# Optimization experiments

Hardware: AMD Instinct MI355X
Metric: run time of the kernel (lower is better)

## Reference

```python
import jax, jax.numpy as jnp
import numpy as np

B, S, D = 2, 2048, 1024  # batch, seq, model_dim
E, K, H = 8, 2, 4096     # experts, top_k, expert hidden
CAP_FACTOR = 1.0


def setup_inputs() -> dict:
    key = jax.random.key(0)
    ks = jax.random.split(key, 6)
    scale_in = 1.0 / np.sqrt(D)
    scale_h = 1.0 / np.sqrt(H)
    return {
        "x": jax.random.normal(ks[0], (B, S, D), jnp.float32),
        "wg": jax.random.normal(ks[1], (D, E), jnp.float32) * scale_in,
        "w1": jax.random.normal(ks[2], (E, D, H), jnp.float32) * scale_in,
        "b1": jnp.zeros((E, H), jnp.float32),
        "w2": jax.random.normal(ks[3], (E, H, D), jnp.float32) * scale_h,
        "b2": jnp.zeros((E, D), jnp.float32),
    }


def _moe_forward(x, wg, w1, b1, w2, b2):
    Bb, Ss, Dd = x.shape
    T = Bb * Ss
    cap = int(K * CAP_FACTOR * ((T + E - 1) // E))  # Tutel capacity rule
    xt = x.reshape(T, Dd)

    # ---- gating ----
    logits = xt @ wg                      # [T, E]
    scores = jax.nn.softmax(logits, axis=-1)
    gates_k, idx_k = jax.lax.top_k(scores, K)  # [T, K]
    # normalize_gate=True: renormalize top-k gates
    gates_k = gates_k / jnp.sum(gates_k, axis=-1, keepdims=True)

    # ---- GShard-style location assignment (slot-major cumsum) ----
    masks = jax.nn.one_hot(idx_k, E, dtype=jnp.int32)           # [T, K, E]
    m = jnp.transpose(masks, (1, 0, 2)).reshape(K * T, E)       # slot-major
    locs_full = jnp.cumsum(m, axis=0) - 1                       # [K*T, E]
    loc = jnp.sum(locs_full * m, axis=-1)                       # [K*T]
    loc = loc.reshape(K, T).T                                   # [T, K]
    valid = (loc < cap).astype(xt.dtype)                        # capacity drop
    loc_c = jnp.clip(loc, 0, cap - 1)

    # ---- dispatch: scatter tokens into [E, cap, D] ----
    contrib = (xt[:, None, :] * valid[:, :, None]).reshape(T * K, Dd)
    disp = jnp.zeros((E, cap, Dd), xt.dtype)
    disp = disp.at[idx_k.reshape(-1), loc_c.reshape(-1)].add(contrib)

    # ---- grouped expert FFN ----
    h = jax.nn.relu(jnp.einsum("ecd,edh->ech", disp, w1) + b1[:, None, :])
    out = jnp.einsum("ech,ehd->ecd", h, w2) + b2[:, None, :]

    # ---- combine (postscore): gather + gate-weighted sum ----
    gathered = out[idx_k, loc_c]                                # [T, K, D]
    y = jnp.einsum("tk,tkd->td", gates_k * valid, gathered)
    return y.reshape(Bb, Ss, Dd)


def reference(x, wg, w1, b1, w2, b2):
    return _moe_forward(x, wg, w1, b1, w2, b2)
```

## Files before the change

### kernel.cpp

```cpp
#include <hip/hip_runtime.h>
#include <stdint.h>

#define NTOK 4096
#define DIM  1024
#define NEXP 8
#define HID  4096
#define CAP  1024

typedef __bf16 bf16x8 __attribute__((ext_vector_type(8)));
typedef float  f32x4  __attribute__((ext_vector_type(4)));

__device__ __forceinline__ unsigned short f2bf(float f) {
  unsigned int u = __float_as_uint(f);
  return (unsigned short)((u + 0x7fffu + ((u >> 16) & 1u)) >> 16);
}

__device__ __forceinline__ float bf2f(unsigned int bits16) {
  return __uint_as_float(bits16 << 16);
}

__device__ __forceinline__ void load_lds16(const void* g, void* l) {
  __builtin_amdgcn_global_load_lds(
      (__attribute__((address_space(1))) void*)g,
      (__attribute__((address_space(3))) void*)l,
      16, 0, 0);
}

__global__ void gating_kernel(const float* __restrict__ x, const float* __restrict__ wg,
                              int* __restrict__ tok_e, float* __restrict__ tok_g) {
  const int t = blockIdx.x;
  const int l = threadIdx.x;
  float acc[NEXP];
#pragma unroll
  for (int e = 0; e < NEXP; ++e) acc[e] = 0.f;

  const float4* x4  = (const float4*)(x + (size_t)t * DIM);
  const float4* wg4 = (const float4*)wg;
#pragma unroll
  for (int i = 0; i < 4; ++i) {
    int dq = i * 64 + l;
    float4 xv = x4[dq];
    float xs[4] = {xv.x, xv.y, xv.z, xv.w};
#pragma unroll
    for (int c = 0; c < 4; ++c) {
      int d = dq * 4 + c;
      float4 wa = wg4[d * 2], wb = wg4[d * 2 + 1];
      acc[0] += xs[c] * wa.x; acc[1] += xs[c] * wa.y;
      acc[2] += xs[c] * wa.z; acc[3] += xs[c] * wa.w;
      acc[4] += xs[c] * wb.x; acc[5] += xs[c] * wb.y;
      acc[6] += xs[c] * wb.z; acc[7] += xs[c] * wb.w;
    }
  }
#pragma unroll
  for (int off = 32; off; off >>= 1)
#pragma unroll
    for (int e = 0; e < NEXP; ++e) acc[e] += __shfl_xor(acc[e], off);

  if (l == 0) {
    float m = acc[0];
#pragma unroll
    for (int e = 1; e < NEXP; ++e) m = fmaxf(m, acc[e]);
    float p[NEXP];
#pragma unroll
    for (int e = 0; e < NEXP; ++e) p[e] = __expf(acc[e] - m);
    int e0 = 0; float b0 = p[0];
#pragma unroll
    for (int e = 1; e < NEXP; ++e) if (p[e] > b0) { b0 = p[e]; e0 = e; }
    int e1 = -1; float b1v = -1.f;
#pragma unroll
    for (int e = 0; e < NEXP; ++e) if (e != e0 && p[e] > b1v) { b1v = p[e]; e1 = e; }
    float inv = 1.f / (b0 + b1v);
    tok_e[2 * t] = e0; tok_e[2 * t + 1] = e1;
    tok_g[2 * t] = b0 * inv; tok_g[2 * t + 1] = b1v * inv;
  }
}

__global__ void scan_kernel(const int* __restrict__ tok_e, int* __restrict__ tok_loc,
                            int* __restrict__ slot_map) {
  const int l = threadIdx.x;
  const unsigned long long below = (1ull << l) - 1ull;
  int base[NEXP];
#pragma unroll
  for (int e = 0; e < NEXP; ++e) base[e] = 0;

  int nxt = tok_e[((0 * 64 + l) & (NTOK - 1)) * 2 + ((0 * 64 + l) >> 12)];
  for (int it = 0; it < 128; ++it) {
    int e = nxt;
    if (it + 1 < 128) {
      int g2 = (it + 1) * 64 + l;
      nxt = tok_e[(g2 & (NTOK - 1)) * 2 + (g2 >> 12)];
    }
    int loc = 0;
#pragma unroll
    for (int ex = 0; ex < NEXP; ++ex) {
      unsigned long long msk = __ballot(e == ex);
      int off = __popcll(msk & below);
      if (e == ex) loc = base[ex] + off;
      base[ex] += __popcll(msk);
    }
    int g = it * 64 + l;
    int k = g >> 12, t = g & (NTOK - 1);
    bool valid = loc < CAP;
    tok_loc[t * 2 + k] = valid ? loc : -1;
    if (valid) slot_map[e * CAP + loc] = t;
  }
#pragma unroll
  for (int ex = 0; ex < NEXP; ++ex) {
    int c = base[ex] < CAP ? base[ex] : CAP;
    for (int i = c + l; i < CAP; i += 64) slot_map[ex * CAP + i] = -1;
  }
}

__global__ void dispatch_kernel(const float* __restrict__ x, const int* __restrict__ slot_map,
                                unsigned short* __restrict__ disp) {
  const int s = blockIdx.x;
  const int tid = threadIdx.x;
  int t = slot_map[s];
  uint2 o;
  if (t >= 0) {
    float4 v = ((const float4*)(x + (size_t)t * DIM))[tid];
    o.x = (unsigned)f2bf(v.x) | ((unsigned)f2bf(v.y) << 16);
    o.y = (unsigned)f2bf(v.z) | ((unsigned)f2bf(v.w) << 16);
  } else {
    o.x = 0u; o.y = 0u;
  }
  ((uint2*)(disp + (size_t)s * DIM))[tid] = o;
}

__global__ void transpose_cvt(const float* __restrict__ in, unsigned short* __restrict__ out,
                              int R, int C) {
  __shared__ float tile[64][65];
  const int e = blockIdx.z;
  const float* inp = in + (size_t)e * R * C;
  unsigned short* outp = out + (size_t)e * R * C;
  const int c0 = blockIdx.x * 64, r0 = blockIdx.y * 64;
  const int t = threadIdx.x;
#pragma unroll
  for (int i = 0; i < 4; ++i) {
    int idx = i * 256 + t;
    int r = idx >> 4, c4 = (idx & 15) * 4;
    float4 v = *(const float4*)(inp + (size_t)(r0 + r) * C + c0 + c4);
    tile[r][c4 + 0] = v.x; tile[r][c4 + 1] = v.y;
    tile[r][c4 + 2] = v.z; tile[r][c4 + 3] = v.w;
  }
  __syncthreads();
#pragma unroll
  for (int i = 0; i < 2; ++i) {
    int idx = i * 256 + t;
    int c = idx >> 3, r8 = (idx & 7) * 8;
    unsigned short s[8];
#pragma unroll
    for (int j = 0; j < 8; ++j) s[j] = f2bf(tile[r8 + j][c]);
    uint4 o;
    o.x = (unsigned)s[0] | ((unsigned)s[1] << 16);
    o.y = (unsigned)s[2] | ((unsigned)s[3] << 16);
    o.z = (unsigned)s[4] | ((unsigned)s[5] << 16);
    o.w = (unsigned)s[6] | ((unsigned)s[7] << 16);
    *(uint4*)(outp + (size_t)(c0 + c) * R + r0 + r8) = o;
  }
}

template <bool RELU, int MB, int NB>
__global__ __launch_bounds__(256)
void gemm_kernel(const unsigned short* __restrict__ A, const unsigned short* __restrict__ B,
                 const float* __restrict__ bias, unsigned short* __restrict__ C,
                 int N, int K) {
  constexpr int M = 1024;
  const int bid = blockIdx.x;
  const int e = bid / (MB * NB);
  const int r = bid - e * (MB * NB);
  const int patch = r / (MB * 4);
  const int q = r - patch * (MB * 4);
  const int mtile = q >> 2;
  const int ntile = patch * 4 + (q & 3);

  A += (size_t)e * M * K;
  B += (size_t)e * N * K;
  bias += (size_t)e * N;
  C += (size_t)e * M * N;
  const int m0 = mtile * 128;
  const int n0 = ntile * 128;
  const int tid = threadIdx.x;
  const int wave = tid >> 6, lane = tid & 63;
  const int wm = wave >> 1, wn = wave & 1;

  __shared__ __align__(16) unsigned short As[128 * 64];
  __shared__ __align__(16) unsigned short Bs[128 * 64];

  const int srow = lane >> 3;
  const int scol = ((lane & 7) ^ (srow & 7)) * 8;
  const unsigned short* gA = A + (size_t)(m0 + wave * 8 + srow) * K + scol;
  const unsigned short* gB = B + (size_t)(n0 + wave * 8 + srow) * K + scol;
  const int lbase = (wave * 8) * 64;

  f32x4 acc[4][4] = {};

  const int quad = lane >> 4;
  const int lxor = lane & 7;
  const int arowb = (wm * 64 + (lane & 15)) * 64;
  const int browb = (wn * 64 + (lane & 15)) * 64;

  const int nIter = K >> 6;
  for (int it = 0; it < nIter; ++it) {
#pragma unroll
    for (int i = 0; i < 4; ++i) {
      load_lds16(gA + (size_t)i * 32 * K, &As[lbase + i * 32 * 64]);
      load_lds16(gB + (size_t)i * 32 * K, &Bs[lbase + i * 32 * 64]);
    }
    gA += 64; gB += 64;
    __syncthreads();
#pragma unroll
    for (int kk = 0; kk < 64; kk += 32) {
      const int coff = ((quad + (kk >> 3)) ^ lxor) * 8;
      bf16x8 af[4], bfr[4];
#pragma unroll
      for (int i = 0; i < 4; ++i)
        af[i] = *reinterpret_cast<const bf16x8*>(&As[arowb + i * 16 * 64 + coff]);
#pragma unroll
      for (int j = 0; j < 4; ++j)
        bfr[j] = *reinterpret_cast<const bf16x8*>(&Bs[browb + j * 16 * 64 + coff]);
#pragma unroll
      for (int i = 0; i < 4; ++i)
#pragma unroll
        for (int j = 0; j < 4; ++j)
          acc[i][j] = __builtin_amdgcn_mfma_f32_16x16x32_bf16(af[i], bfr[j], acc[i][j], 0, 0, 0);
    }
    __syncthreads();
  }

  unsigned short* scr = (wave < 2 ? As : Bs) + (wave & 1) * 2304;
  const int lc = lane & 15;
  const int erow = lane >> 3;
  const int ecol = (lane & 7) * 8;
  unsigned short* Cbase = C + (size_t)(m0 + wm * 64) * N + n0 + wn * 64;
#pragma unroll
  for (int h2 = 0; h2 < 2; ++h2) {
#pragma unroll
    for (int j = 0; j < 4; ++j) {
      float bj = bias[n0 + wn * 64 + j * 16 + lc];
#pragma unroll
      for (int ii = 0; ii < 2; ++ii) {
        int i = h2 * 2 + ii;
#pragma unroll
        for (int rr = 0; rr < 4; ++rr) {
          float v = acc[i][j][rr] + bj;
          if (RELU) v = fmaxf(v, 0.f);
          scr[(ii * 16 + quad * 4 + rr) * 72 + j * 16 + lc] = f2bf(v);
        }
      }
    }
    __asm__ volatile("s_waitcnt lgkmcnt(0)" ::: "memory");
#pragma unroll
    for (int p = 0; p < 4; ++p) {
      uint4 v = *(const uint4*)&scr[(p * 8 + erow) * 72 + ecol];
      *(uint4*)&Cbase[(size_t)(h2 * 32 + p * 8 + erow) * N + ecol] = v;
    }
  }
}

__global__ void combine_kernel(const unsigned short* __restrict__ outb,
                               const int* __restrict__ tok_e, const int* __restrict__ tok_loc,
                               const float* __restrict__ tok_g, float* __restrict__ y) {
  const int t = blockIdx.x;
  const int tid = threadIdx.x;
  int e0 = tok_e[2 * t], e1 = tok_e[2 * t + 1];
  int l0 = tok_loc[2 * t], l1 = tok_loc[2 * t + 1];
  float g0 = tok_g[2 * t], g1 = tok_g[2 * t + 1];
  float ax = 0.f, ay = 0.f, az = 0.f, aw = 0.f;
  if (l0 >= 0) {
    uint2 u = ((const uint2*)(outb + ((size_t)e0 * CAP + l0) * DIM))[tid];
    ax += g0 * bf2f(u.x & 0xffffu); ay += g0 * __uint_as_float(u.x & 0xffff0000u);
    az += g0 * bf2f(u.y & 0xffffu); aw += g0 * __uint_as_float(u.y & 0xffff0000u);
  }
  if (l1 >= 0) {
    uint2 u = ((const uint2*)(outb + ((size_t)e1 * CAP + l1) * DIM))[tid];
    ax += g1 * bf2f(u.x & 0xffffu); ay += g1 * __uint_as_float(u.x & 0xffff0000u);
    az += g1 * bf2f(u.y & 0xffffu); aw += g1 * __uint_as_float(u.y & 0xffff0000u);
  }
  float4 o; o.x = ax; o.y = ay; o.z = az; o.w = aw;
  ((float4*)(y + (size_t)t * DIM))[tid] = o;
}

extern "C" void kernel_launch(void* const* d_in, const int* in_sizes, int n_in,
                              void* d_out, int out_size, void* d_ws, size_t ws_size,
                              hipStream_t stream) {
  const float* x  = (const float*)d_in[0];
  const float* wg = (const float*)d_in[1];
  const float* w1 = (const float*)d_in[2];
  const float* b1 = (const float*)d_in[3];
  const float* w2 = (const float*)d_in[4];
  const float* b2 = (const float*)d_in[5];
  float* y = (float*)d_out;

  char* ws = (char*)d_ws;
  int*   tok_e    = (int*)(ws);
  int*   tok_loc  = (int*)(ws + 32768);
  float* tok_g    = (float*)(ws + 65536);
  int*   slot_map = (int*)(ws + 98304);
  unsigned short* disp = (unsigned short*)(ws + 131072);
  unsigned short* wbuf = (unsigned short*)(ws + 131072 + (16ull << 20));
  unsigned short* h    = (unsigned short*)(ws + 131072 + (80ull << 20));
  unsigned short* outb = (unsigned short*)(ws + 131072 + (144ull << 20));

  gating_kernel<<<NTOK, 64, 0, stream>>>(x, wg, tok_e, tok_g);
  scan_kernel<<<1, 64, 0, stream>>>(tok_e, tok_loc, slot_map);
  dispatch_kernel<<<NEXP * CAP, 256, 0, stream>>>(x, slot_map, disp);
  transpose_cvt<<<dim3(HID / 64, DIM / 64, NEXP), 256, 0, stream>>>(w1, wbuf, DIM, HID);
  gemm_kernel<true, 8, 32><<<NEXP * 8 * 32, 256, 0, stream>>>(disp, wbuf, b1, h, HID, DIM);
  transpose_cvt<<<dim3(DIM / 64, HID / 64, NEXP), 256, 0, stream>>>(w2, wbuf, HID, DIM);
  gemm_kernel<false, 8, 8><<<NEXP * 8 * 8, 256, 0, stream>>>(h, wbuf, b2, outb, DIM, HID);
  combine_kernel<<<NTOK, 256, 0, stream>>>(outb, tok_e, tok_loc, tok_g, y);
}
```

Before: 544.0 us.

## Fuse dispatch and weight fp32-to-bf16 transpose into expert GEMM loads

The separate dispatch kernel and the two weight transpose/convert kernels are removed. Each GEMM now loads fp32 weights directly and converts them to bf16 in registers before writing transposed tiles to LDS, and GEMM1 gathers token rows through slot_map. The scan is split across four waves using per-wave counts and prefix offsets. This avoids writing and re-reading bf16 copies of the weights and dispatched activations. The cost is that each GEMM tile re-reads and re-converts fp32 weights, which doubles global read bytes per tile, and global loads now go through registers with no async LDS path.

Result: slower. 625.3 us (+14.9%).

```diff
diff --git a/kernel.cpp b/kernel.cpp
--- a/kernel.cpp
+++ b/kernel.cpp
@@ -17,6 +17,10 @@
 
 __device__ __forceinline__ float bf2f(unsigned int bits16) {
   return __uint_as_float(bits16 << 16);
+}
+
+__device__ __forceinline__ unsigned packbf(float a, float b) {
+  return __builtin_amdgcn_perm(__float_as_uint(b), __float_as_uint(a), 0x07060302);
 }
 
 __device__ __forceinline__ void load_lds16(const void* g, void* l) {
@@ -77,19 +81,37 @@
 
 __global__ void scan_kernel(const int* __restrict__ tok_e, int* __restrict__ tok_loc,
                             int* __restrict__ slot_map) {
-  const int l = threadIdx.x;
+  __shared__ int wcnt[4][NEXP];
+  const int tid = threadIdx.x;
+  const int w = tid >> 6, l = tid & 63;
   const unsigned long long below = (1ull << l) - 1ull;
+  const int g0 = w * 2048;
+
+  int cnt[NEXP];
+#pragma unroll
+  for (int e = 0; e < NEXP; ++e) cnt[e] = 0;
+  for (int it = 0; it < 32; ++it) {
+    int g = g0 + it * 64 + l;
+    int e = tok_e[(g & (NTOK - 1)) * 2 + (g >> 12)];
+#pragma unroll
+    for (int ex = 0; ex < NEXP; ++ex)
+      cnt[ex] += __popcll(__ballot(e == ex));
+  }
+  if (l == 0)
+#pragma unroll
+    for (int e = 0; e < NEXP; ++e) wcnt[w][e] = cnt[e];
+  __syncthreads();
+
   int base[NEXP];
 #pragma unroll
-  for (int e = 0; e < NEXP; ++e) base[e] = 0;
-
-  int nxt = tok_e[((0 * 64 + l) & (NTOK - 1)) * 2 + ((0 * 64 + l) >> 12)];
-  for (int it = 0; it < 128; ++it) {
-    int e = nxt;
-    if (it + 1 < 128) {
-      int g2 = (it + 1) * 64 + l;
-      nxt = tok_e[(g2 & (NTOK - 1)) * 2 + (g2 >> 12)];
-    }
+  for (int e = 0; e < NEXP; ++e) {
+    int b = 0;
+    for (int w2 = 0; w2 < 4; ++w2) if (w2 < w) b += wcnt[w2][e];
+    base[e] = b;
+  }
+  for (int it = 0; it < 32; ++it) {
+    int g = g0 + it * 64 + l;
+    int e = tok_e[(g & (NTOK - 1)) * 2 + (g >> 12)];
     int loc = 0;
 #pragma unroll
     for (int ex = 0; ex < NEXP; ++ex) {
@@ -98,7 +120,6 @@
       if (e == ex) loc = base[ex] + off;
       base[ex] += __popcll(msk);
     }
-    int g = it * 64 + l;
     int k = g >> 12, t = g & (NTOK - 1);
     bool valid = loc < CAP;
     tok_loc[t * 2 + k] = valid ? loc : -1;
@@ -106,128 +127,104 @@
   }
 #pragma unroll
   for (int ex = 0; ex < NEXP; ++ex) {
-    int c = base[ex] < CAP ? base[ex] : CAP;
-    for (int i = c + l; i < CAP; i += 64) slot_map[ex * CAP + i] = -1;
-  }
-}
-
-__global__ void dispatch_kernel(const float* __restrict__ x, const int* __restrict__ slot_map,
-                                unsigned short* __restrict__ disp) {
-  const int s = blockIdx.x;
-  const int tid = threadIdx.x;
-  int t = slot_map[s];
-  uint2 o;
-  if (t >= 0) {
-    float4 v = ((const float4*)(x + (size_t)t * DIM))[tid];
-    o.x = (unsigned)f2bf(v.x) | ((unsigned)f2bf(v.y) << 16);
-    o.y = (unsigned)f2bf(v.z) | ((unsigned)f2bf(v.w) << 16);
-  } else {
-    o.x = 0u; o.y = 0u;
-  }
-  ((uint2*)(disp + (size_t)s * DIM))[tid] = o;
-}
-
-__global__ void transpose_cvt(const float* __restrict__ in, unsigned short* __restrict__ out,
-                              int R, int C) {
-  __shared__ float tile[64][65];
-  const int e = blockIdx.z;
-  const float* inp = in + (size_t)e * R * C;
-  unsigned short* outp = out + (size_t)e * R * C;
-  const int c0 = blockIdx.x * 64, r0 = blockIdx.y * 64;
-  const int t = threadIdx.x;
-#pragma unroll
-  for (int i = 0; i < 4; ++i) {
-    int idx = i * 256 + t;
-    int r = idx >> 4, c4 = (idx & 15) * 4;
-    float4 v = *(const float4*)(inp + (size_t)(r0 + r) * C + c0 + c4);
-    tile[r][c4 + 0] = v.x; tile[r][c4 + 1] = v.y;
-    tile[r][c4 + 2] = v.z; tile[r][c4 + 3] = v.w;
-  }
-  __syncthreads();
-#pragma unroll
-  for (int i = 0; i < 2; ++i) {
-    int idx = i * 256 + t;
-    int c = idx >> 3, r8 = (idx & 7) * 8;
-    unsigned short s[8];
-#pragma unroll
-    for (int j = 0; j < 8; ++j) s[j] = f2bf(tile[r8 + j][c]);
-    uint4 o;
-    o.x = (unsigned)s[0] | ((unsigned)s[1] << 16);
-    o.y = (unsigned)s[2] | ((unsigned)s[3] << 16);
-    o.z = (unsigned)s[4] | ((unsigned)s[5] << 16);
-    o.w = (unsigned)s[6] | ((unsigned)s[7] << 16);
-    *(uint4*)(outp + (size_t)(c0 + c) * R + r0 + r8) = o;
-  }
-}
-
-template <bool RELU, int MB, int NB>
+    int tot = wcnt[0][ex] + wcnt[1][ex] + wcnt[2][ex] + wcnt[3][ex];
+    int c = tot < CAP ? tot : CAP;
+    for (int i = c + tid; i < CAP; i += 256) slot_map[ex * CAP + i] = -1;
+  }
+}
+
+template <int MB, int NB>
 __global__ __launch_bounds__(256)
-void gemm_kernel(const unsigned short* __restrict__ A, const unsigned short* __restrict__ B,
-                 const float* __restrict__ bias, unsigned short* __restrict__ C,
-                 int N, int K) {
-  constexpr int M = 1024;
+void gemm1_kernel(const float* __restrict__ X, const int* __restrict__ slot_map,
+                  const float* __restrict__ W1, const float* __restrict__ b1,
+                  unsigned short* __restrict__ Hout) {
+  constexpr int M = CAP, N = HID, K = DIM;
   const int bid = blockIdx.x;
   const int e = bid / (MB * NB);
   const int r = bid - e * (MB * NB);
   const int patch = r / (MB * 4);
   const int q = r - patch * (MB * 4);
-  const int mtile = q >> 2;
-  const int ntile = patch * 4 + (q & 3);
-
-  A += (size_t)e * M * K;
-  B += (size_t)e * N * K;
-  bias += (size_t)e * N;
-  C += (size_t)e * M * N;
-  const int m0 = mtile * 128;
-  const int n0 = ntile * 128;
+  const int m0 = (q >> 2) * 128;
+  const int n0 = (patch * 4 + (q & 3)) * 128;
+
+  const float* B = W1 + (size_t)e * K * N;
+  const float* bias = b1 + (size_t)e * N;
+  unsigned short* C = Hout + (size_t)e * M * N;
+
   const int tid = threadIdx.x;
   const int wave = tid >> 6, lane = tid & 63;
   const int wm = wave >> 1, wn = wave & 1;
 
-  __shared__ __align__(16) unsigned short As[128 * 64];
-  __shared__ __align__(16) unsigned short Bs[128 * 64];
-
-  const int srow = lane >> 3;
-  const int scol = ((lane & 7) ^ (srow & 7)) * 8;
-  const unsigned short* gA = A + (size_t)(m0 + wave * 8 + srow) * K + scol;
-  const unsigned short* gB = B + (size_t)(n0 + wave * 8 + srow) * K + scol;
-  const int lbase = (wave * 8) * 64;
+  __shared__ __align__(16) unsigned short As[128 * 72];
+  __shared__ __align__(16) unsigned short Bs[128 * 88];
+
+  const int arow_s = tid >> 1;
+  const int akh = tid & 1;
+  const int t = slot_map[e * CAP + m0 + arow_s];
+  const float* aPtr = X + (size_t)(t < 0 ? 0 : t) * DIM + akh * 32;
+  const bool aValid = (t >= 0);
+  const int bn = 4 * (lane & 31);
+  const int bkb = 16 * wave + 8 * (lane >> 5);
+  const float* bPtr = B + (size_t)bkb * N + n0 + bn;
 
   f32x4 acc[4][4] = {};
-
   const int quad = lane >> 4;
-  const int lxor = lane & 7;
-  const int arowb = (wm * 64 + (lane & 15)) * 64;
-  const int browb = (wn * 64 + (lane & 15)) * 64;
-
-  const int nIter = K >> 6;
-  for (int it = 0; it < nIter; ++it) {
+  const int arowb = (wm * 64 + (lane & 15)) * 72;
+  const int browb = (wn * 64 + (lane & 15)) * 88;
+
+  for (int it = 0; it < K / 64; ++it) {
+    f32x4 fa[8], fb[8];
+#pragma unroll
+    for (int p = 0; p < 8; ++p) fa[p] = *(const f32x4*)(aPtr + p * 4);
+#pragma unroll
+    for (int p = 0; p < 8; ++p) fb[p] = *(const f32x4*)(bPtr + (size_t)p * N);
+    aPtr += 64; bPtr += (size_t)64 * N;
+
+    uint4 wa[4], wb[4];
 #pragma unroll
     for (int i = 0; i < 4; ++i) {
-      load_lds16(gA + (size_t)i * 32 * K, &As[lbase + i * 32 * 64]);
-      load_lds16(gB + (size_t)i * 32 * K, &Bs[lbase + i * 32 * 64]);
-    }
-    gA += 64; gB += 64;
+      f32x4 f0 = fa[2 * i], f1 = fa[2 * i + 1];
+      uint4 u;
+      u.x = packbf(f0[0], f0[1]); u.y = packbf(f0[2], f0[3]);
+      u.z = packbf(f1[0], f1[1]); u.w = packbf(f1[2], f1[3]);
+      if (!aValid) { u.x = 0; u.y = 0; u.z = 0; u.w = 0; }
+      wa[i] = u;
+    }
+#pragma unroll
+    for (int j = 0; j < 4; ++j) {
+      uint4 u;
+      u.x = packbf(fb[0][j], fb[1][j]); u.y = packbf(fb[2][j], fb[3][j]);
+      u.z = packbf(fb[4][j], fb[5][j]); u.w = packbf(fb[6][j], fb[7][j]);
+      wb[j] = u;
+    }
+
     __syncthreads();
 #pragma unroll
+    for (int i = 0; i < 4; ++i)
+      *(uint4*)&As[arow_s * 72 + akh * 32 + i * 8] = wa[i];
+#pragma unroll
+    for (int j = 0; j < 4; ++j)
+      *(uint4*)&Bs[(bn + j) * 88 + (bkb >> 3) * 8] = wb[j];
+    __syncthreads();
+
+#pragma unroll
     for (int kk = 0; kk < 64; kk += 32) {
-      const int coff = ((quad + (kk >> 3)) ^ lxor) * 8;
       bf16x8 af[4], bfr[4];
 #pragma unroll
       for (int i = 0; i < 4; ++i)
-        af[i] = *reinterpret_cast<const bf16x8*>(&As[arowb + i * 16 * 64 + coff]);
+        af[i] = *reinterpret_cast<const bf16x8*>(&As[arowb + i * 16 * 72 + quad * 8 + kk]);
 #pragma unroll
       for (int j = 0; j < 4; ++j)
-        bfr[j] = *reinterpret_cast<const bf16x8*>(&Bs[browb + j * 16 * 64 + coff]);
+        bfr[j] = *reinterpret_cast<const bf16x8*>(&Bs[browb + j * 16 * 88 + quad * 8 + kk]);
 #pragma unroll
       for (int i = 0; i < 4; ++i)
 #pragma unroll
         for (int j = 0; j < 4; ++j)
           acc[i][j] = __builtin_amdgcn_mfma_f32_16x16x32_bf16(af[i], bfr[j], acc[i][j], 0, 0, 0);
     }
-    __syncthreads();
-  }
-
+  }
+
+  __syncthreads();
   unsigned short* scr = (wave < 2 ? As : Bs) + (wave & 1) * 2304;
   const int lc = lane & 15;
   const int erow = lane >> 3;
@@ -243,8 +240,118 @@
         int i = h2 * 2 + ii;
 #pragma unroll
         for (int rr = 0; rr < 4; ++rr) {
+          float v = fmaxf(acc[i][j][rr] + bj, 0.f);
+          scr[(ii * 16 + quad * 4 + rr) * 72 + j * 16 + lc] = f2bf(v);
+        }
+      }
+    }
+    __asm__ volatile("s_waitcnt lgkmcnt(0)" ::: "memory");
+#pragma unroll
+    for (int p = 0; p < 4; ++p) {
+      uint4 v = *(const uint4*)&scr[(p * 8 + erow) * 72 + ecol];
+      *(uint4*)&Cbase[(size_t)(h2 * 32 + p * 8 + erow) * N + ecol] = v;
+    }
+  }
+}
+
+template <int MB, int NB>
+__global__ __launch_bounds__(256)
+void gemm2_kernel(const unsigned short* __restrict__ Hin, const float* __restrict__ W2,
+                  const float* __restrict__ b2, unsigned short* __restrict__ Out) {
+  constexpr int M = CAP, N = DIM, K = HID;
+  const int bid = blockIdx.x;
+  const int e = bid / (MB * NB);
+  const int r = bid - e * (MB * NB);
+  const int patch = r / (MB * 4);
+  const int q = r - patch * (MB * 4);
+  const int m0 = (q >> 2) * 128;
+  const int n0 = (patch * 4 + (q & 3)) * 128;
+
+  const unsigned short* A = Hin + (size_t)e * M * K;
+  const float* B = W2 + (size_t)e * K * N;
+  const float* bias = b2 + (size_t)e * N;
+  unsigned short* C = Out + (size_t)e * M * N;
+
+  const int tid = threadIdx.x;
+  const int wave = tid >> 6, lane = tid & 63;
+  const int wm = wave >> 1, wn = wave & 1;
+
+  __shared__ __align__(16) unsigned short As[128 * 64];
+  __shared__ __align__(16) unsigned short Bs[128 * 88];
+
+  const int srow = lane >> 3;
+  const int scol = ((lane & 7) ^ (srow & 7)) * 8;
+  const unsigned short* gA = A + (size_t)(m0 + wave * 8 + srow) * K + scol;
+  const int lbase = (wave * 8) * 64;
+  const int bn = 4 * (lane & 31);
+  const int bkb = 16 * wave + 8 * (lane >> 5);
+  const float* bPtr = B + (size_t)bkb * N + n0 + bn;
+
+  f32x4 acc[4][4] = {};
+  const int quad = lane >> 4;
+  const int lxor = lane & 7;
+  const int arowb = (wm * 64 + (lane & 15)) * 64;
+  const int browb = (wn * 64 + (lane & 15)) * 88;
+
+  for (int it = 0; it < K / 64; ++it) {
+    f32x4 fb[8];
+#pragma unroll
+    for (int p = 0; p < 8; ++p) fb[p] = *(const f32x4*)(bPtr + (size_t)p * N);
+    bPtr += (size_t)64 * N;
+    uint4 wb[4];
+#pragma unroll
+    for (int j = 0; j < 4; ++j) {
+      uint4 u;
+      u.x = packbf(fb[0][j], fb[1][j]); u.y = packbf(fb[2][j], fb[3][j]);
+      u.z = packbf(fb[4][j], fb[5][j]); u.w = packbf(fb[6][j], fb[7][j]);
+      wb[j] = u;
+    }
+
+    __syncthreads();
+#pragma unroll
+    for (int i = 0; i < 4; ++i)
+      load_lds16(gA + (size_t)i * 32 * K, &As[lbase + i * 32 * 64]);
+    gA += 64;
+#pragma unroll
+    for (int j = 0; j < 4; ++j)
+      *(uint4*)&Bs[(bn + j) * 88 + (bkb >> 3) * 8] = wb[j];
+    __syncthreads();
+
+#pragma unroll
+    for (int kk = 0; kk < 64; kk += 32) {
+      const int coff = ((quad + (kk >> 3)) ^ lxor) * 8;
+      bf16x8 af[4], bfr[4];
+#pragma unroll
+      for (int i = 0; i < 4; ++i)
+        af[i] = *reinterpret_cast<const bf16x8*>(&As[arowb + i * 16 * 64 + coff]);
+#pragma unroll
+      for (int j = 0; j < 4; ++j)
+        bfr[j] = *reinterpret_cast<const bf16x8*>(&Bs[browb + j * 16 * 88 + quad * 8 + kk]);
+#pragma unroll
+      for (int i = 0; i < 4; ++i)
+#pragma unroll
+        for (int j = 0; j < 4; ++j)
+          acc[i][j] = __builtin_amdgcn_mfma_f32_16x16x32_bf16(af[i], bfr[j], acc[i][j], 0, 0, 0);
+    }
+  }
+
+  __syncthreads();
+  unsigned short* scr = (wave < 2 ? As : Bs) + (wave & 1) * 2304;
+  const int lc = lane & 15;
+  const int erow = lane >> 3;
+  const int ecol = (lane & 7) * 8;
+  unsigned short* Cbase = C + (size_t)(m0 + wm * 64) * N + n0 + wn * 64;
+#pragma unroll
+  for (int h2 = 0; h2 < 2; ++h2) {
+#pragma unroll
+    for (int j = 0; j < 4; ++j) {
+      float bj = bias[n0 + wn * 64 + j * 16 + lc];
+#pragma unroll
+      for (int ii = 0; ii < 2; ++ii) {
+        int i = h2 * 2 + ii;
+#pragma unroll
+        for (int rr = 0; rr < 4; ++rr) {
           float v = acc[i][j][rr] + bj;
-          if (RELU) v = fmaxf(v, 0.f);
           scr[(ii * 16 + quad * 4 + rr) * 72 + j * 16 + lc] = f2bf(v);
         }
       }
@@ -297,17 +404,12 @@
   int*   tok_loc  = (int*)(ws + 32768);
   float* tok_g    = (float*)(ws + 65536);
   int*   slot_map = (int*)(ws + 98304);
-  unsigned short* disp = (unsigned short*)(ws + 131072);
-  unsigned short* wbuf = (unsigned short*)(ws + 131072 + (16ull << 20));
-  unsigned short* h    = (unsigned short*)(ws + 131072 + (80ull << 20));
-  unsigned short* outb = (unsigned short*)(ws + 131072 + (144ull << 20));
+  unsigned short* h    = (unsigned short*)(ws + 131072);
+  unsigned short* outb = (unsigned short*)(ws + 131072 + (64ull << 20));
 
   gating_kernel<<<NTOK, 64, 0, stream>>>(x, wg, tok_e, tok_g);
-  scan_kernel<<<1, 64, 0, stream>>>(tok_e, tok_loc, slot_map);
-  dispatch_kernel<<<NEXP * CAP, 256, 0, stream>>>(x, slot_map, disp);
-  transpose_cvt<<<dim3(HID / 64, DIM / 64, NEXP), 256, 0, stream>>>(w1, wbuf, DIM, HID);
-  gemm_kernel<true, 8, 32><<<NEXP * 8 * 32, 256, 0, stream>>>(disp, wbuf, b1, h, HID, DIM);
-  transpose_cvt<<<dim3(DIM / 64, HID / 64, NEXP), 256, 0, stream>>>(w2, wbuf, HID, DIM);
-  gemm_kernel<false, 8, 8><<<NEXP * 8 * 8, 256, 0, stream>>>(h, wbuf, b2, outb, DIM, HID);
+  scan_kernel<<<1, 256, 0, stream>>>(tok_e, tok_loc, slot_map);
+  gemm1_kernel<8, 32><<<NEXP * 8 * 32, 256, 0, stream>>>(x, slot_map, w1, b1, h);
+  gemm2_kernel<8, 8><<<NEXP * 8 * 8, 256, 0, stream>>>(h, w2, b2, outb);
   combine_kernel<<<NTOK, 256, 0, stream>>>(outb, tok_e, tok_loc, tok_g, y);
 }
```
